# Performance work log

Measured on AMD Instinct MI355X. Metric: run time of the kernel, lower is better.

## Reference

```python
import jax, jax.numpy as jnp
import numpy as np

N_NODES = 50000
N_EDGES = 800000
NUM_GRAPHS = 128

def _sage_conv(x, src, dst, Wl, b, Wr):
    # PyG SAGEConv: lin_l(mean_{j in N(i)} x_j) + lin_r(x_i); bias only on lin_l
    msgs = x[src]                                             # [E, d] gather
    agg = jax.ops.segment_sum(msgs, dst, num_segments=N_NODES)
    deg = jax.ops.segment_sum(jnp.ones((src.shape[0],), x.dtype), dst,
                              num_segments=N_NODES)
    mean = agg / jnp.maximum(deg, 1.0)[:, None]               # [N, d]
    return mean @ Wl.T + b + x @ Wr.T

def setup_inputs() -> dict:
    key = jax.random.key(0)
    ks = jax.random.split(key, 12)
    d_in, d_h, d_out = 96, 96, 64
    def w(k, o, i):
        return jax.random.normal(k, (o, i), jnp.float32) * (1.0 / np.sqrt(i))
    return {
        "x": jax.random.normal(ks[0], (N_NODES, d_in), jnp.float32),
        "edge_index": jax.random.randint(ks[1], (2, N_EDGES), 0, N_NODES, jnp.int32),
        "batch": jnp.sort(jax.random.randint(ks[2], (N_NODES,), 0, NUM_GRAPHS, jnp.int32)),
        "Wl0": w(ks[3], d_h, d_in), "b0": jnp.zeros((d_h,), jnp.float32), "Wr0": w(ks[4], d_h, d_in),
        "Wl1": w(ks[5], d_h, d_h),  "b1": jnp.zeros((d_h,), jnp.float32), "Wr1": w(ks[6], d_h, d_h),
        "Wl2": w(ks[7], d_out, d_h), "b2": jnp.zeros((d_out,), jnp.float32), "Wr2": w(ks[8], d_out, d_h),
    }

def reference(x, edge_index, batch, Wl0, b0, Wr0, Wl1, b1, Wr1, Wl2, b2, Wr2):
    src, dst = edge_index[0], edge_index[1]
    h = jax.nn.relu(_sage_conv(x, src, dst, Wl0, b0, Wr0))   # dropout: eval mode -> identity
    h = jax.nn.relu(_sage_conv(h, src, dst, Wl1, b1, Wr1))
    h = _sage_conv(h, src, dst, Wl2, b2, Wr2)                 # [N, out]
    # global_mean_pool over graphs
    pooled = jax.ops.segment_sum(h, batch, num_segments=NUM_GRAPHS)
    cnt = jax.ops.segment_sum(jnp.ones((h.shape[0],), h.dtype), batch,
                              num_segments=NUM_GRAPHS)
    return pooled / jnp.maximum(cnt, 1.0)[:, None]            # [num_graphs, out]
```

## Files before the change

kernel.cpp:

```cpp
#include <hip/hip_runtime.h>
#include <stdint.h>
#include <stddef.h>

#define NN 50000
#define NP 50048
#define NE 800000
#define NG 128

#define NBKT 256
#define NPB 196
#define BCAP 4096
#define TILE_E 3200

typedef __attribute__((ext_vector_type(8))) short bf16x8;
typedef __attribute__((ext_vector_type(4))) float f32x4;
typedef unsigned short ushort_t;
typedef unsigned int uint_t;

static __device__ inline ushort_t f2b(float f) {
    union { float f; uint_t u; } v; v.f = f;
    uint_t r = v.u + 0x7FFFu + ((v.u >> 16) & 1u);
    return (ushort_t)(r >> 16);
}
static __device__ inline float blo(uint_t u) {
    union { uint_t u; float f; } v; v.u = u << 16; return v.f;
}
static __device__ inline float bhi(uint_t u) {
    union { uint_t u; float f; } v; v.u = u & 0xFFFF0000u; return v.f;
}

static __global__ void cvt_zero_kernel(const float* __restrict__ x, ushort_t* __restrict__ xb,
                                       int* __restrict__ bucket_cnt, int* __restrict__ cnt,
                                       float* __restrict__ accum) {
    int gid = blockIdx.x * 256 + threadIdx.x;
    if (gid < NBKT) bucket_cnt[gid] = 0;
    if (gid < NG) cnt[gid] = 0;
    if (gid < NG * 64) accum[gid] = 0.f;
    int i = gid * 4;
    if (i + 3 < NN * 96) {
        float4 v = *(const float4*)(x + i);
        ushort_t o0 = f2b(v.x), o1 = f2b(v.y), o2 = f2b(v.z), o3 = f2b(v.w);
        uint_t lo = (uint_t)o0 | ((uint_t)o1 << 16);
        uint_t hi = (uint_t)o2 | ((uint_t)o3 << 16);
        *(uint2*)(xb + i) = make_uint2(lo, hi);
    }
}

__launch_bounds__(256) static __global__
void partition_kernel(const int* __restrict__ src, const int* __restrict__ dst,
                      int* __restrict__ bucket_cnt, uint_t* __restrict__ part) {
    __shared__ int hist[NBKT];
    int tid = threadIdx.x;
    hist[tid] = 0;
    __syncthreads();
    int base = blockIdx.x * TILE_E;
    uint_t pk[TILE_E / 256 + 1];
    int bk[TILE_E / 256 + 1];
    int cnt = 0;
    for (int i = base + tid; i < base + TILE_E; i += 256) {
        int s = src[i], d = dst[i];
        int b = d / NPB;
        int dl = d - b * NPB;
        pk[cnt] = ((uint_t)dl << 16) | (uint_t)s;
        bk[cnt] = b;
        cnt++;
        atomicAdd(&hist[b], 1);
    }
    __syncthreads();
    int r = atomicAdd(&bucket_cnt[tid], hist[tid]);
    __syncthreads();
    hist[tid] = r;
    __syncthreads();
    for (int j = 0; j < cnt; j++) {
        int p = atomicAdd(&hist[bk[j]], 1);
        part[bk[j] * BCAP + p] = pk[j];
    }
}

__launch_bounds__(256) static __global__
void csr_build_kernel(const uint_t* __restrict__ part, const int* __restrict__ bucket_cnt,
                      int* __restrict__ deg, int* __restrict__ offs, int* __restrict__ csr) {
    __shared__ uint_t stage[BCAP];
    __shared__ ushort_t cstage[BCAP];
    __shared__ int cnt_s[NBKT];
    __shared__ int scan_l[NBKT];
    __shared__ int cur_l[NBKT];
    int b = blockIdx.x, tid = threadIdx.x;
    int bc = bucket_cnt[tid];
    cnt_s[tid] = bc;
    scan_l[tid] = bc;
    __syncthreads();
    for (int off = 1; off < NBKT; off <<= 1) {
        int t = (tid >= off) ? scan_l[tid - off] : 0;
        __syncthreads();
        scan_l[tid] += t;
        __syncthreads();
    }
    int base = scan_l[b] - cnt_s[b];
    int n = cnt_s[b];
    __syncthreads();
    cnt_s[tid] = 0;
    __syncthreads();
    for (int i = tid; i < n; i += 256) {
        uint_t e = part[(size_t)b * BCAP + i];
        stage[i] = e;
        atomicAdd(&cnt_s[e >> 16], 1);
    }
    __syncthreads();
    int v = cnt_s[tid];
    scan_l[tid] = v;
    __syncthreads();
    for (int off = 1; off < NBKT; off <<= 1) {
        int t = (tid >= off) ? scan_l[tid - off] : 0;
        __syncthreads();
        scan_l[tid] += t;
        __syncthreads();
    }
    int ex = scan_l[tid] - v;
    scan_l[tid] = ex;
    cur_l[tid] = 0;
    __syncthreads();
    int g = b * NPB + tid;
    if (tid < NPB && g < NN) { deg[g] = v; offs[g] = base + ex; }
    for (int i = tid; i < n; i += 256) {
        uint_t e = stage[i];
        int dl = e >> 16;
        int p = atomicAdd(&cur_l[dl], 1);
        cstage[scan_l[dl] + p] = (ushort_t)(e & 0xFFFFu);
    }
    __syncthreads();
    for (int i = tid; i < n; i += 256) csr[base + i] = (int)cstage[i];
}

template <int DOUT, int NT>
__launch_bounds__(256, 4) static __global__
void transform_kernel(const ushort_t* __restrict__ hb, const float* __restrict__ Wl,
                      const float* __restrict__ bias, const float* __restrict__ Wr,
                      ushort_t* __restrict__ tlb, ushort_t* __restrict__ trb) {
    constexpr int DIN = 96;
    __shared__ short w_s[NT * 3 * 64 * 8];
    int tid = threadIdx.x;
    for (int idx = tid; idx < NT * 3 * 64; idx += 256) {
        int ci = idx >> 6, ln = idx & 63;
        int t = ci / 3, s = ci - 3 * t;
        int o = t * 16 + (ln & 15);
        int c0 = s * 32 + (ln >> 4) * 8;
        const float* wrow = (o < DOUT) ? (Wl + (size_t)o * DIN)
                                       : (Wr + (size_t)(o - DOUT) * DIN);
        float4 v0 = *(const float4*)(wrow + c0);
        float4 v1 = *(const float4*)(wrow + c0 + 4);
        bf16x8 pk;
        pk[0] = (short)f2b(v0.x); pk[1] = (short)f2b(v0.y);
        pk[2] = (short)f2b(v0.z); pk[3] = (short)f2b(v0.w);
        pk[4] = (short)f2b(v1.x); pk[5] = (short)f2b(v1.y);
        pk[6] = (short)f2b(v1.z); pk[7] = (short)f2b(v1.w);
        *(bf16x8*)&w_s[idx * 8] = pk;
    }
    int lane = tid & 63;
    int m0 = blockIdx.x * 64 + (tid >> 6) * 16;
    int row = m0 + (lane & 15);
    const bf16x8* arow = (const bf16x8*)(hb + (size_t)row * DIN) + (lane >> 4);
    bf16x8 a0 = arow[0];
    bf16x8 a1 = arow[4];
    bf16x8 a2 = arow[8];
    __syncthreads();
    const bf16x8* wp = (const bf16x8*)w_s + lane;
    f32x4 acc[NT];
#pragma unroll
    for (int t = 0; t < NT; t++) {
        acc[t] = (f32x4){0.f, 0.f, 0.f, 0.f};
        acc[t] = __builtin_amdgcn_mfma_f32_16x16x32_bf16(a0, wp[(t * 3 + 0) * 64], acc[t], 0, 0, 0);
        acc[t] = __builtin_amdgcn_mfma_f32_16x16x32_bf16(a1, wp[(t * 3 + 1) * 64], acc[t], 0, 0, 0);
        acc[t] = __builtin_amdgcn_mfma_f32_16x16x32_bf16(a2, wp[(t * 3 + 2) * 64], acc[t], 0, 0, 0);
    }
    int quad = lane >> 4, col = lane & 15;
#pragma unroll
    for (int t = 0; t < NT; t++) {
        int o = t * 16 + col;
        bool is_r = (o >= DOUT);
        float bv = is_r ? bias[o - DOUT] : 0.f;
        ushort_t* outp = is_r ? trb : tlb;
        int oo = is_r ? (o - DOUT) : o;
#pragma unroll
        for (int r = 0; r < 4; r++) {
            int node = m0 + quad * 4 + r;
            if (node < NN) outp[(size_t)node * DOUT + oo] = f2b(acc[t][r] + bv);
        }
    }
}

template <int D, bool RELU, bool OUT_BF16>
static __global__ void agg2_kernel(const ushort_t* __restrict__ tlb, const ushort_t* __restrict__ trb,
                                   const int* __restrict__ offs, const int* __restrict__ deg,
                                   const int* __restrict__ csr, void* __restrict__ outv) {
    constexpr int RD = D / 2;
    constexpr int AL = D / 8;
    int gtid = blockIdx.x * 256 + threadIdx.x;
    int node = gtid >> 4;
    int lane = threadIdx.x & 15;
    if (node >= NN) return;
    int ll = (lane < AL) ? lane : 0;
    int off = offs[node], dg = deg[node];
    const uint_t* tl32 = (const uint_t*)tlb;
    float acc[8];
#pragma unroll
    for (int q = 0; q < 8; q++) acc[q] = 0.f;
    int k = 0;
    for (; k + 4 <= dg; k += 4) {
        int i0 = csr[off + k + 0];
        int i1 = csr[off + k + 1];
        int i2 = csr[off + k + 2];
        int i3 = csr[off + k + 3];
        uint4 a0 = *(const uint4*)(tl32 + (size_t)i0 * RD + 4 * ll);
        uint4 a1 = *(const uint4*)(tl32 + (size_t)i1 * RD + 4 * ll);
        uint4 a2 = *(const uint4*)(tl32 + (size_t)i2 * RD + 4 * ll);
        uint4 a3 = *(const uint4*)(tl32 + (size_t)i3 * RD + 4 * ll);
        acc[0] += (blo(a0.x) + blo(a1.x)) + (blo(a2.x) + blo(a3.x));
        acc[1] += (bhi(a0.x) + bhi(a1.x)) + (bhi(a2.x) + bhi(a3.x));
        acc[2] += (blo(a0.y) + blo(a1.y)) + (blo(a2.y) + blo(a3.y));
        acc[3] += (bhi(a0.y) + bhi(a1.y)) + (bhi(a2.y) + bhi(a3.y));
        acc[4] += (blo(a0.z) + blo(a1.z)) + (blo(a2.z) + blo(a3.z));
        acc[5] += (bhi(a0.z) + bhi(a1.z)) + (bhi(a2.z) + bhi(a3.z));
        acc[6] += (blo(a0.w) + blo(a1.w)) + (blo(a2.w) + blo(a3.w));
        acc[7] += (bhi(a0.w) + bhi(a1.w)) + (bhi(a2.w) + bhi(a3.w));
    }
    for (; k < dg; k++) {
        uint4 a0 = *(const uint4*)(tl32 + (size_t)csr[off + k] * RD + 4 * ll);
        acc[0] += blo(a0.x); acc[1] += bhi(a0.x);
        acc[2] += blo(a0.y); acc[3] += bhi(a0.y);
        acc[4] += blo(a0.z); acc[5] += bhi(a0.z);
        acc[6] += blo(a0.w); acc[7] += bhi(a0.w);
    }
    float s = 1.f / (float)max(dg, 1);
    uint4 t = *(const uint4*)((const uint_t*)trb + (size_t)node * RD + 4 * ll);
    float v0 = fmaf(acc[0], s, blo(t.x));
    float v1 = fmaf(acc[1], s, bhi(t.x));
    float v2 = fmaf(acc[2], s, blo(t.y));
    float v3 = fmaf(acc[3], s, bhi(t.y));
    float v4 = fmaf(acc[4], s, blo(t.z));
    float v5 = fmaf(acc[5], s, bhi(t.z));
    float v6 = fmaf(acc[6], s, blo(t.w));
    float v7 = fmaf(acc[7], s, bhi(t.w));
    if (RELU) {
        v0 = fmaxf(v0, 0.f); v1 = fmaxf(v1, 0.f); v2 = fmaxf(v2, 0.f); v3 = fmaxf(v3, 0.f);
        v4 = fmaxf(v4, 0.f); v5 = fmaxf(v5, 0.f); v6 = fmaxf(v6, 0.f); v7 = fmaxf(v7, 0.f);
    }
    if (lane < AL) {
        if (OUT_BF16) {
            uint4 o;
            o.x = (uint_t)f2b(v0) | ((uint_t)f2b(v1) << 16);
            o.y = (uint_t)f2b(v2) | ((uint_t)f2b(v3) << 16);
            o.z = (uint_t)f2b(v4) | ((uint_t)f2b(v5) << 16);
            o.w = (uint_t)f2b(v6) | ((uint_t)f2b(v7) << 16);
            *(uint4*)((uint_t*)outv + (size_t)node * RD + 4 * lane) = o;
        } else {
            float* op = (float*)outv + (size_t)node * D + 8 * lane;
            *(float4*)op = make_float4(v0, v1, v2, v3);
            *(float4*)(op + 4) = make_float4(v4, v5, v6, v7);
        }
    }
}

static __global__ void pool_kernel(const float* __restrict__ h, const int* __restrict__ batch,
                                   float* __restrict__ accum, int* __restrict__ cnt) {
    int per = (NN + gridDim.x - 1) / gridDim.x;
    int start = blockIdx.x * per;
    int end = min(start + per, NN);
    if (start >= end) return;
    int c = threadIdx.x;
    int gcur = batch[start];
    float acc = 0.f;
    int count = 0;
    for (int i = start; i < end; i++) {
        int g = batch[i];
        if (g != gcur) {
            atomicAdd(&accum[gcur * 64 + c], acc);
            if (c == 0) atomicAdd(&cnt[gcur], count);
            acc = 0.f; count = 0; gcur = g;
        }
        acc += h[(size_t)i * 64 + c];
        count++;
    }
    atomicAdd(&accum[gcur * 64 + c], acc);
    if (c == 0) atomicAdd(&cnt[gcur], count);
}

static __global__ void finalize_kernel(const float* __restrict__ accum, const int* __restrict__ cnt,
                                       float* __restrict__ out) {
    int i = blockIdx.x * 256 + threadIdx.x;
    if (i < NG * 64) {
        int g = i >> 6;
        out[i] = accum[i] / (float)max(cnt[g], 1);
    }
}

extern "C" void kernel_launch(void* const* d_in, const int* in_sizes, int n_in,
                              void* d_out, int out_size, void* d_ws, size_t ws_size,
                              hipStream_t stream) {
    (void)in_sizes; (void)n_in; (void)out_size; (void)ws_size;
    const float* x   = (const float*)d_in[0];
    const int*   ei  = (const int*)d_in[1];
    const int*   bat = (const int*)d_in[2];
    const float* Wl0 = (const float*)d_in[3];
    const float* b0  = (const float*)d_in[4];
    const float* Wr0 = (const float*)d_in[5];
    const float* Wl1 = (const float*)d_in[6];
    const float* b1  = (const float*)d_in[7];
    const float* Wr1 = (const float*)d_in[8];
    const float* Wl2 = (const float*)d_in[9];
    const float* b2  = (const float*)d_in[10];
    const float* Wr2 = (const float*)d_in[11];
    float* out = (float*)d_out;
    const int* src = ei;
    const int* dst = ei + NE;

    char* p = (char*)d_ws;
    auto carve = [&](size_t bytes) -> char* {
        char* r = p;
        p += (bytes + 255) & ~(size_t)255;
        return r;
    };
    int*      deg    = (int*)carve((size_t)NN * 4);
    int*      offs   = (int*)carve((size_t)NN * 4);
    int*      bucket_cnt = (int*)carve(NBKT * 4);
    uint_t*   part   = (uint_t*)carve((size_t)NBKT * BCAP * 4);
    int*      csr    = (int*)carve((size_t)NE * 4);
    int*      cnt    = (int*)carve(NG * 4);
    float*    accum  = (float*)carve((size_t)NG * 64 * 4);
    ushort_t* xb     = (ushort_t*)carve((size_t)NP * 96 * 2);
    ushort_t* h1b    = (ushort_t*)carve((size_t)NP * 96 * 2);
    ushort_t* tlb    = (ushort_t*)carve((size_t)NP * 96 * 2);
    ushort_t* trb    = (ushort_t*)carve((size_t)NP * 96 * 2);
    float*    Hf     = (float*)carve((size_t)NN * 64 * 4);

    dim3 b256(256);
    cvt_zero_kernel<<<dim3((NN * 96 / 4 + 255) / 256), b256, 0, stream>>>(x, xb, bucket_cnt, cnt, accum);

    partition_kernel<<<dim3(NE / TILE_E), b256, 0, stream>>>(src, dst, bucket_cnt, part);
    csr_build_kernel<<<dim3(NBKT), b256, 0, stream>>>(part, bucket_cnt, deg, offs, csr);

    dim3 tGrid(NP / 64);
    dim3 aGrid(NN * 16 / 256);

    transform_kernel<96, 12><<<tGrid, b256, 0, stream>>>(xb, Wl0, b0, Wr0, tlb, trb);
    agg2_kernel<96, true, true><<<aGrid, b256, 0, stream>>>(tlb, trb, offs, deg, csr, h1b);
    transform_kernel<96, 12><<<tGrid, b256, 0, stream>>>(h1b, Wl1, b1, Wr1, tlb, trb);
    agg2_kernel<96, true, true><<<aGrid, b256, 0, stream>>>(tlb, trb, offs, deg, csr, xb);
    transform_kernel<64, 8><<<tGrid, b256, 0, stream>>>(xb, Wl2, b2, Wr2, tlb, trb);
    agg2_kernel<64, false, false><<<aGrid, b256, 0, stream>>>(tlb, trb, offs, deg, csr, Hf);

    pool_kernel<<<dim3(512), dim3(64), 0, stream>>>(Hf, bat, accum, cnt);
    finalize_kernel<<<dim3((NG * 64 + 255) / 256), b256, 0, stream>>>(accum, cnt, out);
}
```

Baseline: 270.0 us.

## Chunk transformed features into 32-column slabs and aggregate per chunk

The transform kernel now writes its outputs in a chunked layout, with 32 features per chunk stored contiguously per node. The aggregation kernel runs one grid slice per chunk, so each 64-byte neighbour row lands in a smaller per-chunk working set that caches better. Within each 16-lane node group, four sub-groups process different neighbours in parallel and combine their sums with shuffles, and no lanes sit idle. The partition kernel is also changed to read edges twice instead of buffering them in registers, and the pool grid is doubled. The costs are more blocks, extra shuffle reductions, and duplicate reads of dst in partitioning.

```diff
diff --git a/kernel.cpp b/kernel.cpp
--- a/kernel.cpp
+++ b/kernel.cpp
@@ -10,7 +10,8 @@
 #define NBKT 256
 #define NPB 196
 #define BCAP 4096
-#define TILE_E 3200
+#define TILE_E 3072
+#define AGB 3125
 
 typedef __attribute__((ext_vector_type(8))) short bf16x8;
 typedef __attribute__((ext_vector_type(4))) float f32x4;
@@ -54,26 +55,20 @@
     hist[tid] = 0;
     __syncthreads();
     int base = blockIdx.x * TILE_E;
-    uint_t pk[TILE_E / 256 + 1];
-    int bk[TILE_E / 256 + 1];
-    int cnt = 0;
-    for (int i = base + tid; i < base + TILE_E; i += 256) {
+    int end = min(base + TILE_E, NE);
+    for (int i = base + tid; i < end; i += 256)
+        atomicAdd(&hist[dst[i] / NPB], 1);
+    __syncthreads();
+    int r = atomicAdd(&bucket_cnt[tid], hist[tid]);
+    __syncthreads();
+    hist[tid] = r;
+    __syncthreads();
+    for (int i = base + tid; i < end; i += 256) {
         int s = src[i], d = dst[i];
         int b = d / NPB;
         int dl = d - b * NPB;
-        pk[cnt] = ((uint_t)dl << 16) | (uint_t)s;
-        bk[cnt] = b;
-        cnt++;
-        atomicAdd(&hist[b], 1);
-    }
-    __syncthreads();
-    int r = atomicAdd(&bucket_cnt[tid], hist[tid]);
-    __syncthreads();
-    hist[tid] = r;
-    __syncthreads();
-    for (int j = 0; j < cnt; j++) {
-        int p = atomicAdd(&hist[bk[j]], 1);
-        part[bk[j] * BCAP + p] = pk[j];
+        int p = atomicAdd(&hist[b], 1);
+        part[b * BCAP + p] = ((uint_t)dl << 16) | (uint_t)s;
     }
 }
 
@@ -136,7 +131,7 @@
 __launch_bounds__(256, 4) static __global__
 void transform_kernel(const ushort_t* __restrict__ hb, const float* __restrict__ Wl,
                       const float* __restrict__ bias, const float* __restrict__ Wr,
-                      ushort_t* __restrict__ tlb, ushort_t* __restrict__ trb) {
+                      ushort_t* __restrict__ tlc, ushort_t* __restrict__ trc) {
     constexpr int DIN = 96;
     __shared__ short w_s[NT * 3 * 64 * 8];
     int tid = threadIdx.x;
@@ -179,60 +174,70 @@
         int o = t * 16 + col;
         bool is_r = (o >= DOUT);
         float bv = is_r ? bias[o - DOUT] : 0.f;
-        ushort_t* outp = is_r ? trb : tlb;
+        ushort_t* outp = is_r ? trc : tlc;
         int oo = is_r ? (o - DOUT) : o;
+        int cch = oo >> 5, f = oo & 31;
+        ushort_t* ob = outp + ((size_t)cch * NN) * 32 + f;
 #pragma unroll
         for (int r = 0; r < 4; r++) {
             int node = m0 + quad * 4 + r;
-            if (node < NN) outp[(size_t)node * DOUT + oo] = f2b(acc[t][r] + bv);
+            if (node < NN) ob[(size_t)node * 32] = f2b(acc[t][r] + bv);
         }
     }
 }
 
 template <int D, bool RELU, bool OUT_BF16>
-static __global__ void agg2_kernel(const ushort_t* __restrict__ tlb, const ushort_t* __restrict__ trb,
-                                   const int* __restrict__ offs, const int* __restrict__ deg,
-                                   const int* __restrict__ csr, void* __restrict__ outv) {
-    constexpr int RD = D / 2;
-    constexpr int AL = D / 8;
-    int gtid = blockIdx.x * 256 + threadIdx.x;
-    int node = gtid >> 4;
-    int lane = threadIdx.x & 15;
-    if (node >= NN) return;
-    int ll = (lane < AL) ? lane : 0;
+__launch_bounds__(256) static __global__
+void agg3_kernel(const ushort_t* __restrict__ tlc, const ushort_t* __restrict__ trc,
+                 const int* __restrict__ offs, const int* __restrict__ deg,
+                 const int* __restrict__ csr, void* __restrict__ outv) {
+    int bx = blockIdx.x;
+    int c = bx / AGB;
+    int b = bx - c * AGB;
+    int tid = threadIdx.x;
+    int node = b * 16 + (tid >> 4);
+    int lane = tid & 15;
+    int ng = lane >> 2, fl = lane & 3;
+    const uint_t* tl = (const uint_t*)tlc + (size_t)c * NN * 16;
     int off = offs[node], dg = deg[node];
-    const uint_t* tl32 = (const uint_t*)tlb;
     float acc[8];
 #pragma unroll
     for (int q = 0; q < 8; q++) acc[q] = 0.f;
     int k = 0;
-    for (; k + 4 <= dg; k += 4) {
-        int i0 = csr[off + k + 0];
-        int i1 = csr[off + k + 1];
-        int i2 = csr[off + k + 2];
-        int i3 = csr[off + k + 3];
-        uint4 a0 = *(const uint4*)(tl32 + (size_t)i0 * RD + 4 * ll);
-        uint4 a1 = *(const uint4*)(tl32 + (size_t)i1 * RD + 4 * ll);
-        uint4 a2 = *(const uint4*)(tl32 + (size_t)i2 * RD + 4 * ll);
-        uint4 a3 = *(const uint4*)(tl32 + (size_t)i3 * RD + 4 * ll);
-        acc[0] += (blo(a0.x) + blo(a1.x)) + (blo(a2.x) + blo(a3.x));
-        acc[1] += (bhi(a0.x) + bhi(a1.x)) + (bhi(a2.x) + bhi(a3.x));
-        acc[2] += (blo(a0.y) + blo(a1.y)) + (blo(a2.y) + blo(a3.y));
-        acc[3] += (bhi(a0.y) + bhi(a1.y)) + (bhi(a2.y) + bhi(a3.y));
-        acc[4] += (blo(a0.z) + blo(a1.z)) + (blo(a2.z) + blo(a3.z));
-        acc[5] += (bhi(a0.z) + bhi(a1.z)) + (bhi(a2.z) + bhi(a3.z));
-        acc[6] += (blo(a0.w) + blo(a1.w)) + (blo(a2.w) + blo(a3.w));
-        acc[7] += (bhi(a0.w) + bhi(a1.w)) + (bhi(a2.w) + bhi(a3.w));
-    }
-    for (; k < dg; k++) {
-        uint4 a0 = *(const uint4*)(tl32 + (size_t)csr[off + k] * RD + 4 * ll);
+    for (; k + 8 <= dg; k += 8) {
+        int s0 = csr[off + k + ng];
+        int s1 = csr[off + k + 4 + ng];
+        uint4 a0 = *(const uint4*)(tl + (size_t)s0 * 16 + 4 * fl);
+        uint4 a1 = *(const uint4*)(tl + (size_t)s1 * 16 + 4 * fl);
+        acc[0] += blo(a0.x) + blo(a1.x); acc[1] += bhi(a0.x) + bhi(a1.x);
+        acc[2] += blo(a0.y) + blo(a1.y); acc[3] += bhi(a0.y) + bhi(a1.y);
+        acc[4] += blo(a0.z) + blo(a1.z); acc[5] += bhi(a0.z) + bhi(a1.z);
+        acc[6] += blo(a0.w) + blo(a1.w); acc[7] += bhi(a0.w) + bhi(a1.w);
+    }
+    if (k + 4 <= dg) {
+        int s0 = csr[off + k + ng];
+        uint4 a0 = *(const uint4*)(tl + (size_t)s0 * 16 + 4 * fl);
         acc[0] += blo(a0.x); acc[1] += bhi(a0.x);
         acc[2] += blo(a0.y); acc[3] += bhi(a0.y);
         acc[4] += blo(a0.z); acc[5] += bhi(a0.z);
         acc[6] += blo(a0.w); acc[7] += bhi(a0.w);
+        k += 4;
+    }
+    if (ng < dg - k) {
+        int s0 = csr[off + k + ng];
+        uint4 a0 = *(const uint4*)(tl + (size_t)s0 * 16 + 4 * fl);
+        acc[0] += blo(a0.x); acc[1] += bhi(a0.x);
+        acc[2] += blo(a0.y); acc[3] += bhi(a0.y);
+        acc[4] += blo(a0.z); acc[5] += bhi(a0.z);
+        acc[6] += blo(a0.w); acc[7] += bhi(a0.w);
+    }
+#pragma unroll
+    for (int q = 0; q < 8; q++) {
+        acc[q] += __shfl_xor(acc[q], 4, 64);
+        acc[q] += __shfl_xor(acc[q], 8, 64);
     }
     float s = 1.f / (float)max(dg, 1);
-    uint4 t = *(const uint4*)((const uint_t*)trb + (size_t)node * RD + 4 * ll);
+    uint4 t = *(const uint4*)((const uint_t*)trc + (size_t)c * NN * 16 + (size_t)node * 16 + 4 * fl);
     float v0 = fmaf(acc[0], s, blo(t.x));
     float v1 = fmaf(acc[1], s, bhi(t.x));
     float v2 = fmaf(acc[2], s, blo(t.y));
@@ -245,16 +250,16 @@
         v0 = fmaxf(v0, 0.f); v1 = fmaxf(v1, 0.f); v2 = fmaxf(v2, 0.f); v3 = fmaxf(v3, 0.f);
         v4 = fmaxf(v4, 0.f); v5 = fmaxf(v5, 0.f); v6 = fmaxf(v6, 0.f); v7 = fmaxf(v7, 0.f);
     }
-    if (lane < AL) {
+    if (ng == 0) {
         if (OUT_BF16) {
             uint4 o;
             o.x = (uint_t)f2b(v0) | ((uint_t)f2b(v1) << 16);
             o.y = (uint_t)f2b(v2) | ((uint_t)f2b(v3) << 16);
             o.z = (uint_t)f2b(v4) | ((uint_t)f2b(v5) << 16);
             o.w = (uint_t)f2b(v6) | ((uint_t)f2b(v7) << 16);
-            *(uint4*)((uint_t*)outv + (size_t)node * RD + 4 * lane) = o;
+            *(uint4*)((uint_t*)outv + (size_t)node * (D / 2) + c * 16 + 4 * fl) = o;
         } else {
-            float* op = (float*)outv + (size_t)node * D + 8 * lane;
+            float* op = (float*)outv + (size_t)node * D + c * 32 + 8 * fl;
             *(float4*)op = make_float4(v0, v1, v2, v3);
             *(float4*)(op + 4) = make_float4(v4, v5, v6, v7);
         }
@@ -329,26 +334,25 @@
     float*    accum  = (float*)carve((size_t)NG * 64 * 4);
     ushort_t* xb     = (ushort_t*)carve((size_t)NP * 96 * 2);
     ushort_t* h1b    = (ushort_t*)carve((size_t)NP * 96 * 2);
-    ushort_t* tlb    = (ushort_t*)carve((size_t)NP * 96 * 2);
-    ushort_t* trb    = (ushort_t*)carve((size_t)NP * 96 * 2);
+    ushort_t* tlc    = (ushort_t*)carve((size_t)3 * NN * 32 * 2);
+    ushort_t* trc    = (ushort_t*)carve((size_t)3 * NN * 32 * 2);
     float*    Hf     = (float*)carve((size_t)NN * 64 * 4);
 
     dim3 b256(256);
     cvt_zero_kernel<<<dim3((NN * 96 / 4 + 255) / 256), b256, 0, stream>>>(x, xb, bucket_cnt, cnt, accum);
 
-    partition_kernel<<<dim3(NE / TILE_E), b256, 0, stream>>>(src, dst, bucket_cnt, part);
+    partition_kernel<<<dim3((NE + TILE_E - 1) / TILE_E), b256, 0, stream>>>(src, dst, bucket_cnt, part);
     csr_build_kernel<<<dim3(NBKT), b256, 0, stream>>>(part, bucket_cnt, deg, offs, csr);
 
     dim3 tGrid(NP / 64);
-    dim3 aGrid(NN * 16 / 256);
-
-    transform_kernel<96, 12><<<tGrid, b256, 0, stream>>>(xb, Wl0, b0, Wr0, tlb, trb);
-    agg2_kernel<96, true, true><<<aGrid, b256, 0, stream>>>(tlb, trb, offs, deg, csr, h1b);
-    transform_kernel<96, 12><<<tGrid, b256, 0, stream>>>(h1b, Wl1, b1, Wr1, tlb, trb);
-    agg2_kernel<96, true, true><<<aGrid, b256, 0, stream>>>(tlb, trb, offs, deg, csr, xb);
-    transform_kernel<64, 8><<<tGrid, b256, 0, stream>>>(xb, Wl2, b2, Wr2, tlb, trb);
-    agg2_kernel<64, false, false><<<aGrid, b256, 0, stream>>>(tlb, trb, offs, deg, csr, Hf);
-
-    pool_kernel<<<dim3(512), dim3(64), 0, stream>>>(Hf, bat, accum, cnt);
+
+    transform_kernel<96, 12><<<tGrid, b256, 0, stream>>>(xb, Wl0, b0, Wr0, tlc, trc);
+    agg3_kernel<96, true, true><<<dim3(3 * AGB), b256, 0, stream>>>(tlc, trc, offs, deg, csr, h1b);
+    transform_kernel<96, 12><<<tGrid, b256, 0, stream>>>(h1b, Wl1, b1, Wr1, tlc, trc);
+    agg3_kernel<96, true, true><<<dim3(3 * AGB), b256, 0, stream>>>(tlc, trc, offs, deg, csr, xb);
+    transform_kernel<64, 8><<<tGrid, b256, 0, stream>>>(xb, Wl2, b2, Wr2, tlc, trc);
+    agg3_kernel<64, false, false><<<dim3(2 * AGB), b256, 0, stream>>>(tlc, trc, offs, deg, csr, Hf);
+
+    pool_kernel<<<dim3(1024), dim3(64), 0, stream>>>(Hf, bat, accum, cnt);
     finalize_kernel<<<dim3((NG * 64 + 255) / 256), b256, 0, stream>>>(accum, cnt, out);
 }
```

After: 261.3 us. -3.2%, faster.
